# Optimization experiments

Measured on AMD Instinct MI355X. Metric: run time of the kernel, lower is better.

Reference implementation:

```python
import jax, jax.numpy as jnp
import numpy as np
from jax import lax

K = 9      # 3x3 kernel points
PAD = 1
EPS = 1e-5

def _conv3x3(x, w):
    # x: [B,C,H,W], w: [O,C,3,3] -> [B,O,H,W], stride 1, pad 1
    return lax.conv_general_dilated(x, w, (1, 1), [(PAD, PAD), (PAD, PAD)],
                                    dimension_numbers=('NCHW', 'OIHW', 'NCHW'))

def _bilinear_sample(x, py, px):
    # x: [B,C,H,W]; py,px: [B,K,H,W] float sample coords -> [B,C,K,H,W]
    # Zero padding outside bounds (mmcv deform_conv semantics).
    B, C, H, W = x.shape
    y0 = jnp.floor(py)
    x0 = jnp.floor(px)
    wy1 = py - y0
    wx1 = px - x0
    xf = x.reshape(B, C, H * W)

    def corner(yc, xc, wgt):
        valid = (yc >= 0) & (yc <= H - 1) & (xc >= 0) & (xc <= W - 1)
        yi = jnp.clip(yc, 0, H - 1).astype(jnp.int32)
        xi = jnp.clip(xc, 0, W - 1).astype(jnp.int32)
        idx = (yi * W + xi).reshape(B, -1)                       # [B, K*H*W]
        v = jax.vmap(lambda f, i: jnp.take(f, i, axis=1))(xf, idx)  # [B,C,K*H*W]
        v = v.reshape(B, C, K, H, W)
        return v * jnp.where(valid, wgt, 0.0)[:, None]

    return (corner(y0,     x0,     (1 - wy1) * (1 - wx1))
          + corner(y0,     x0 + 1, (1 - wy1) * wx1)
          + corner(y0 + 1, x0,     wy1 * (1 - wx1))
          + corner(y0 + 1, x0 + 1, wy1 * wx1))

def _dcn_bn_relu(x, w_off, b_off, w, gamma, beta, mean, var):
    B, C, H, W = x.shape
    # offset conv: [B, 2K, H, W]; channel pairs are (dy, dx) per kernel point
    off = _conv3x3(x, w_off) + b_off[None, :, None, None]
    off = off.reshape(B, K, 2, H, W)
    dy, dx = off[:, :, 0], off[:, :, 1]
    kk = jnp.arange(K)
    ky = (kk // 3 - PAD).astype(x.dtype)   # kernel y deltas
    kx = (kk % 3 - PAD).astype(x.dtype)    # kernel x deltas
    py = dy + jnp.arange(H, dtype=x.dtype)[None, None, :, None] + ky[None, :, None, None]
    px = dx + jnp.arange(W, dtype=x.dtype)[None, None, None, :] + kx[None, :, None, None]
    s = _bilinear_sample(x, py, px)                       # [B,C,K,H,W]
    out = jnp.einsum('bckhw,ock->bohw', s, w.reshape(w.shape[0], C, K))
    # BatchNorm (eval stats) + ReLU
    inv = gamma * lax.rsqrt(var + EPS)
    return jax.nn.relu(out * inv[None, :, None, None]
                       + (beta - mean * inv)[None, :, None, None])

def setup_inputs() -> dict:
    key = jax.random.key(0)
    ks = jax.random.split(key, 8)
    B, Cin, Cout, H, W = 4, 64, 64, 128, 128
    fan = 1.0 / np.sqrt(Cin * K)
    return {
        'x':      jax.random.normal(ks[0], (B, Cin, H, W), jnp.float32),
        'w_off1': jax.random.normal(ks[1], (2 * K, Cin, 3, 3), jnp.float32) * 0.1,
        'b_off1': jnp.zeros((2 * K,), jnp.float32),
        'w1':     jax.random.normal(ks[2], (Cout, Cin, 3, 3), jnp.float32) * fan,
        'g1':     jnp.ones((Cout,), jnp.float32),
        'be1':    jnp.zeros((Cout,), jnp.float32),
        'm1':     jax.random.normal(ks[3], (Cout,), jnp.float32) * 0.01,
        'v1':     jnp.abs(jax.random.normal(ks[4], (Cout,), jnp.float32)) * 0.1 + 0.9,
        'w_off2': jax.random.normal(ks[5], (2 * K, Cout, 3, 3), jnp.float32) * 0.1,
        'b_off2': jnp.zeros((2 * K,), jnp.float32),
        'w2':     jax.random.normal(ks[6], (Cout, Cout, 3, 3), jnp.float32) * fan,
        'g2':     jnp.ones((Cout,), jnp.float32),
        'be2':    jnp.zeros((Cout,), jnp.float32),
        'm2':     jax.random.normal(ks[7], (Cout,), jnp.float32) * 0.01,
        'v2':     jnp.ones((Cout,), jnp.float32),
    }

def reference(x, w_off1, b_off1, w1, g1, be1, m1, v1,
              w_off2, b_off2, w2, g2, be2, m2, v2):
    h = _dcn_bn_relu(x, w_off1, b_off1, w1, g1, be1, m1, v1)
    return _dcn_bn_relu(h, w_off2, b_off2, w2, g2, be2, m2, v2)
```

## Files before the change

kernel.cpp:

```cpp
#include <hip/hip_runtime.h>

#define BAR_LGKM()                                         \
  do {                                                     \
    asm volatile("s_waitcnt lgkmcnt(0)" ::: "memory");     \
    __builtin_amdgcn_s_barrier();                          \
  } while (0)

__device__ __forceinline__ int swz_block(int bid) {
  return ((bid & 7) << 7) + (bid >> 3);
}


__global__ __launch_bounds__(256) void prep_kernel(
    const float* __restrict__ w1, const float* __restrict__ w2,
    const float* __restrict__ woff1, const float* __restrict__ woff2,
    const float* __restrict__ g1, const float* __restrict__ be1,
    const float* __restrict__ m1, const float* __restrict__ v1,
    const float* __restrict__ g2, const float* __restrict__ be2,
    const float* __restrict__ m2, const float* __restrict__ v2,
    float* __restrict__ ws) {
  float* wt1 = ws;
  float* wt2 = ws + 36864;
  float* wo1 = ws + 73728;
  float* wo2 = ws + 84096;
  float* bn1 = ws + 94464;
  float* bn2 = ws + 94592;
  int idx = blockIdx.x * 256 + threadIdx.x;
  if (idx < 73728) {
    int t = (idx < 36864) ? idx : idx - 36864;
    const float* w = (idx < 36864) ? w1 : w2;
    float* wt = (idx < 36864) ? wt1 : wt2;
    int oi = t & 7;
    int rest = t >> 3;
    int k = rest % 9;
    int cog = rest / 9;
    int og = cog & 7, c = cog >> 3;
    int o = og * 8 + oi;
    wt[t] = w[(o * 64 + c) * 9 + k];
  } else if (idx < 94464) {
    int u = idx - 73728;
    int t2 = (u < 10368) ? u : u - 10368;
    const float* w = (u < 10368) ? woff1 : woff2;
    float* wo = (u < 10368) ? wo1 : wo2;
    int j = t2 % 18;
    int v = t2 / 18;
    int tt = v % 9;
    int c = v / 9;
    wo[t2] = w[(j * 64 + c) * 9 + tt];
  } else if (idx < 94528) {
    int o = idx - 94464;
    float s = g1[o] * rsqrtf(v1[o] + 1e-5f);
    bn1[o] = s;
    bn1[64 + o] = be1[o] - m1[o] * s;
  } else if (idx < 94592) {
    int o = idx - 94528;
    float s = g2[o] * rsqrtf(v2[o] + 1e-5f);
    bn2[o] = s;
    bn2[64 + o] = be2[o] - m2[o] * s;
  }
}

__global__ __launch_bounds__(512, 8) void conv_off_kernel(
    const float* __restrict__ xin, const float* __restrict__ wofft,
    const float* __restrict__ boff, float* __restrict__ off) {
  __shared__ float halo[2][792];
  int tid = threadIdx.x;
  int pxl = tid & 63;
  int og = tid >> 6;
  int ogu = __builtin_amdgcn_readfirstlane(og);
  int p0 = swz_block(blockIdx.x) * 64;
  int b = p0 >> 14, hw0 = p0 & 16383;
  int h = hw0 >> 7, w0 = hw0 & 127;

  bool sv = tid < 396;
  int pp = (tid >= 198) ? 1 : 0;
  int pos = tid - pp * 198;
  int r = pos / 66, cc = pos - r * 66;
  int yy = h + r - 1, xx = w0 + cc - 1;
  bool inb = sv && (yy >= 0) && (yy < 128) && (xx >= 0) && (xx < 128);
  int ofs = (yy << 7) + xx;
  const float* xb0 = xin + ((size_t)(b * 64) << 14);

  float stg0 = inb ? xb0[((size_t)pp << 14) + ofs] : 0.f;
  float stg1 = inb ? xb0[((size_t)(2 + pp) << 14) + ofs] : 0.f;

  int jbase = (ogu < 2) ? ogu * 3 : 6 + (ogu - 2) * 2;
  int nj = (ogu < 2) ? 3 : 2;
  int jc2 = jbase + 2;
  if (jc2 > 17) jc2 = 17;

  float acc[3] = {0.f, 0.f, 0.f};

#pragma unroll 1
  for (int cg = 0; cg < 64; cg += 4) {
    int bufi = (cg >> 2) & 1;
    if (sv) {
      halo[bufi][pp * 198 + pos] = stg0;
      halo[bufi][(2 + pp) * 198 + pos] = stg1;
    }
    if (cg < 60) {
      stg0 = inb ? xb0[((size_t)(cg + 4 + pp) << 14) + ofs] : 0.f;
      stg1 = inb ? xb0[((size_t)(cg + 6 + pp) << 14) + ofs] : 0.f;
    }
    BAR_LGKM();
    const float* hb = halo[bufi];
#pragma unroll
    for (int p = 0; p < 4; ++p) {
      const float* wc = wofft + (cg + p) * 162;
#pragma unroll
      for (int t = 0; t < 9; ++t) {
        float v = hb[p * 198 + (t / 3) * 66 + pxl + (t % 3)];
        acc[0] = fmaf(v, wc[t * 18 + jbase], acc[0]);
        acc[1] = fmaf(v, wc[t * 18 + jbase + 1], acc[1]);
        acc[2] = fmaf(v, wc[t * 18 + jc2], acc[2]);
      }
    }
  }
#pragma unroll
  for (int i = 0; i < 3; ++i) {
    if (i < nj) {
      int j = jbase + i;
      off[((size_t)(b * 18 + j) << 14) + hw0 + pxl] = acc[i] + boff[j];
    }
  }
}

__global__ __launch_bounds__(512, 8) void dcn_main_kernel(
    const float* __restrict__ xin, const float* __restrict__ off,
    const float* __restrict__ wt, const float* __restrict__ bn,
    float* __restrict__ out) {
  __shared__ float sbuf[2][576];
  int tid = threadIdx.x;
  int pxl = tid & 63;
  int og = tid >> 6;
  int ogu = __builtin_amdgcn_readfirstlane(og);
  int p0 = swz_block(blockIdx.x) * 64;
  int b = p0 >> 14, hw0 = p0 & 16383;
  int h = hw0 >> 7, w0 = hw0 & 127;
  const float* xb = xin + ((size_t)b << 20);

  bool act1 = (tid & 7) == 0;
  int s1 = 512 + (tid >> 3);

  float pw0[4], pw1[4];
  int ra0, rb0, ra1, rb1;
  bool se0a, se1a, se0b, se1b;

#pragma unroll
  for (int j = 0; j < 2; ++j) {
    bool a = (j == 0) || act1;
    int s = (j == 0) ? tid : s1;
    int k = s >> 6;
    int pxs = s & 63;
    int hw = hw0 + pxs;
    float dy = a ? off[((size_t)(b * 18 + 2 * k) << 14) + hw] : 0.f;
    float dx = a ? off[((size_t)(b * 18 + 2 * k + 1) << 14) + hw] : 0.f;
    float py = (float)(h + k / 3 - 1) + dy;
    float pxf = (float)(w0 + pxs + k % 3 - 1) + dx;
    float y0f = floorf(py), x0f = floorf(pxf);
    float wy1 = py - y0f, wx1 = pxf - x0f;
    float wy0 = 1.f - wy1, wx0 = 1.f - wx1;
    int y0 = (int)y0f, x0 = (int)x0f;
    int y1 = y0 + 1, x1 = x0 + 1;
    bool vy0 = (y0 >= 0) && (y0 <= 127);
    bool vy1 = (y1 >= 0) && (y1 <= 127);
    bool vx0 = (x0 >= 0) && (x0 <= 127);
    bool vx1 = (x1 >= 0) && (x1 <= 127);
    float* pw = (j == 0) ? pw0 : pw1;
    pw[0] = (vy0 && vx0) ? wy0 * wx0 : 0.f;
    pw[1] = (vy0 && vx1) ? wy0 * wx1 : 0.f;
    pw[2] = (vy1 && vx0) ? wy1 * wx0 : 0.f;
    pw[3] = (vy1 && vx1) ? wy1 * wx1 : 0.f;
    int y0c = min(max(y0, 0), 127), y1c = min(max(y1, 0), 127);
    int xb2 = min(max(x0, 0), 126);
    if (j == 0) {
      ra0 = (y0c << 7) + xb2; rb0 = (y1c << 7) + xb2;
      se0a = (x0 == xb2); se1a = (x0 + 1 == xb2);
    } else {
      ra1 = (y0c << 7) + xb2; rb1 = (y1c << 7) + xb2;
      se0b = (x0 == xb2); se1b = (x0 + 1 == xb2);
    }
  }

  float2 A0, A1, A2, A3, B0, B1, B2, B3;
  A0 = *(const float2*)(xb + ra0);
  A1 = *(const float2*)(xb + rb0);
  A2 = act1 ? *(const float2*)(xb + ra1) : make_float2(0.f, 0.f);
  A3 = act1 ? *(const float2*)(xb + rb1) : make_float2(0.f, 0.f);
  {
    const float* x1p = xb + 16384;
    B0 = *(const float2*)(x1p + ra0);
    B1 = *(const float2*)(x1p + rb0);
    B2 = act1 ? *(const float2*)(x1p + ra1) : make_float2(0.f, 0.f);
    B3 = act1 ? *(const float2*)(x1p + rb1) : make_float2(0.f, 0.f);
  }

  float acc[8];
#pragma unroll
  for (int oi = 0; oi < 8; ++oi) acc[oi] = 0.f;

#pragma unroll 1
  for (int c = 0; c < 64; c += 2) {
    {
      float v00 = se0a ? A0.x : A0.y;
      float v01 = se1a ? A0.x : A0.y;
      float v10 = se0a ? A1.x : A1.y;
      float v11 = se1a ? A1.x : A1.y;
      sbuf[0][tid] = fmaf(pw0[0], v00,
                     fmaf(pw0[1], v01,
                     fmaf(pw0[2], v10, pw0[3] * v11)));
    }
    if (act1) {
      float v00 = se0b ? A2.x : A2.y;
      float v01 = se1b ? A2.x : A2.y;
      float v10 = se0b ? A3.x : A3.y;
      float v11 = se1b ? A3.x : A3.y;
      sbuf[0][s1] = fmaf(pw1[0], v00,
                    fmaf(pw1[1], v01,
                    fmaf(pw1[2], v10, pw1[3] * v11)));
    }
    if (c < 62) {
      const float* xn = xb + ((size_t)(c + 2) << 14);
      A0 = *(const float2*)(xn + ra0);
      A1 = *(const float2*)(xn + rb0);
      if (act1) {
        A2 = *(const float2*)(xn + ra1);
        A3 = *(const float2*)(xn + rb1);
      }
    }
    BAR_LGKM();
    {
      const float* wc = wt + (c * 8 + ogu) * 72;
#pragma unroll
      for (int k = 0; k < 9; ++k) {
        float sval = sbuf[0][k * 64 + pxl];
#pragma unroll
        for (int oi = 0; oi < 8; ++oi)
          acc[oi] = fmaf(sval, wc[k * 8 + oi], acc[oi]);
      }
    }
    {
      float v00 = se0a ? B0.x : B0.y;
      float v01 = se1a ? B0.x : B0.y;
      float v10 = se0a ? B1.x : B1.y;
      float v11 = se1a ? B1.x : B1.y;
      sbuf[1][tid] = fmaf(pw0[0], v00,
                     fmaf(pw0[1], v01,
                     fmaf(pw0[2], v10, pw0[3] * v11)));
    }
    if (act1) {
      float v00 = se0b ? B2.x : B2.y;
      float v01 = se1b ? B2.x : B2.y;
      float v10 = se0b ? B3.x : B3.y;
      float v11 = se1b ? B3.x : B3.y;
      sbuf[1][s1] = fmaf(pw1[0], v00,
                    fmaf(pw1[1], v01,
                    fmaf(pw1[2], v10, pw1[3] * v11)));
    }
    if (c < 61) {
      const float* xn = xb + ((size_t)(c + 3) << 14);
      B0 = *(const float2*)(xn + ra0);
      B1 = *(const float2*)(xn + rb0);
      if (act1) {
        B2 = *(const float2*)(xn + ra1);
        B3 = *(const float2*)(xn + rb1);
      }
    }
    BAR_LGKM();
    {
      const float* wc = wt + ((c + 1) * 8 + ogu) * 72;
#pragma unroll
      for (int k = 0; k < 9; ++k) {
        float sval = sbuf[1][k * 64 + pxl];
#pragma unroll
        for (int oi = 0; oi < 8; ++oi)
          acc[oi] = fmaf(sval, wc[k * 8 + oi], acc[oi]);
      }
    }
  }

#pragma unroll
  for (int oi = 0; oi < 8; ++oi) {
    int o = ogu * 8 + oi;
    float rres = fmaf(acc[oi], bn[o], bn[64 + o]);
    out[((size_t)(b * 64 + o) << 14) + hw0 + pxl] = fmaxf(rres, 0.f);
  }
}

extern "C" void kernel_launch(void* const* d_in, const int* in_sizes, int n_in,
                              void* d_out, int out_size, void* d_ws, size_t ws_size,
                              hipStream_t stream) {
  const float* x      = (const float*)d_in[0];
  const float* w_off1 = (const float*)d_in[1];
  const float* b_off1 = (const float*)d_in[2];
  const float* w1     = (const float*)d_in[3];
  const float* g1     = (const float*)d_in[4];
  const float* be1    = (const float*)d_in[5];
  const float* m1     = (const float*)d_in[6];
  const float* v1     = (const float*)d_in[7];
  const float* w_off2 = (const float*)d_in[8];
  const float* b_off2 = (const float*)d_in[9];
  const float* w2     = (const float*)d_in[10];
  const float* g2     = (const float*)d_in[11];
  const float* be2    = (const float*)d_in[12];
  const float* m2     = (const float*)d_in[13];
  const float* v2     = (const float*)d_in[14];
  float* out = (float*)d_out;

  float* ws   = (float*)d_ws;
  float* wt1  = ws;
  float* wt2  = ws + 36864;
  float* wo1  = ws + 73728;
  float* wo2  = ws + 84096;
  float* bn1  = ws + 94464;
  float* bn2  = ws + 94592;
  float* offb = ws + 94720;
  float* hbuf = ws + 1274368;

  prep_kernel<<<370, 256, 0, stream>>>(w1, w2, w_off1, w_off2,
                                       g1, be1, m1, v1, g2, be2, m2, v2, ws);

  conv_off_kernel<<<1024, 512, 0, stream>>>(x, wo1, b_off1, offb);
  dcn_main_kernel<<<1024, 512, 0, stream>>>(x, offb, wt1, bn1, hbuf);

  conv_off_kernel<<<1024, 512, 0, stream>>>(hbuf, wo2, b_off2, offb);
  dcn_main_kernel<<<1024, 512, 0, stream>>>(hbuf, offb, wt2, bn2, out);
}
```

Baseline: 386.9 us.

## Stage weights in LDS and merge channel pairs into one barrier per iteration

The main DCN kernel now double-buffers both the sampled values and the per-channel-pair weights in shared memory. Two channels are processed per iteration with one barrier instead of two. Weights are prefetched into registers and staged cooperatively, replacing the per-wave scalar global weight loads with float4 LDS reads. This cuts barrier count and scalar memory latency, at the cost of more LDS and more registers, which may lower occupancy under launch bounds of 512 threads with 8 blocks.

```diff
diff --git a/kernel.cpp b/kernel.cpp
--- a/kernel.cpp
+++ b/kernel.cpp
@@ -129,7 +129,8 @@
     const float* __restrict__ xin, const float* __restrict__ off,
     const float* __restrict__ wt, const float* __restrict__ bn,
     float* __restrict__ out) {
-  __shared__ float sbuf[2][576];
+  __shared__ __align__(16) float sS[2][1152];
+  __shared__ __align__(16) float sW[2][1152];
   int tid = threadIdx.x;
   int pxl = tid & 63;
   int og = tid >> 6;
@@ -141,6 +142,7 @@
 
   bool act1 = (tid & 7) == 0;
   int s1 = 512 + (tid >> 3);
+  bool wl = tid < 288;
 
   float pw0[4], pw1[4];
   int ra0, rb0, ra1, rb1;
@@ -194,6 +196,7 @@
     B2 = act1 ? *(const float2*)(x1p + ra1) : make_float2(0.f, 0.f);
     B3 = act1 ? *(const float2*)(x1p + rb1) : make_float2(0.f, 0.f);
   }
+  float4 wreg = wl ? *(const float4*)(wt + (tid << 2)) : make_float4(0, 0, 0, 0);
 
   float acc[8];
 #pragma unroll
@@ -201,23 +204,39 @@
 
 #pragma unroll 1
   for (int c = 0; c < 64; c += 2) {
+    int buf = (c >> 1) & 1;
+    if (wl) *(float4*)&sW[buf][tid << 2] = wreg;
     {
       float v00 = se0a ? A0.x : A0.y;
       float v01 = se1a ? A0.x : A0.y;
       float v10 = se0a ? A1.x : A1.y;
       float v11 = se1a ? A1.x : A1.y;
-      sbuf[0][tid] = fmaf(pw0[0], v00,
+      sS[buf][tid] = fmaf(pw0[0], v00,
                      fmaf(pw0[1], v01,
                      fmaf(pw0[2], v10, pw0[3] * v11)));
+      v00 = se0a ? B0.x : B0.y;
+      v01 = se1a ? B0.x : B0.y;
+      v10 = se0a ? B1.x : B1.y;
+      v11 = se1a ? B1.x : B1.y;
+      sS[buf][576 + tid] = fmaf(pw0[0], v00,
+                           fmaf(pw0[1], v01,
+                           fmaf(pw0[2], v10, pw0[3] * v11)));
     }
     if (act1) {
       float v00 = se0b ? A2.x : A2.y;
       float v01 = se1b ? A2.x : A2.y;
       float v10 = se0b ? A3.x : A3.y;
       float v11 = se1b ? A3.x : A3.y;
-      sbuf[0][s1] = fmaf(pw1[0], v00,
+      sS[buf][s1] = fmaf(pw1[0], v00,
                     fmaf(pw1[1], v01,
                     fmaf(pw1[2], v10, pw1[3] * v11)));
+      v00 = se0b ? B2.x : B2.y;
+      v01 = se1b ? B2.x : B2.y;
+      v10 = se0b ? B3.x : B3.y;
+      v11 = se1b ? B3.x : B3.y;
+      sS[buf][576 + s1] = fmaf(pw1[0], v00,
+                          fmaf(pw1[1], v01,
+                          fmaf(pw1[2], v10, pw1[3] * v11)));
     }
     if (c < 62) {
       const float* xn = xb + ((size_t)(c + 2) << 14);
@@ -227,54 +246,33 @@
         A2 = *(const float2*)(xn + ra1);
         A3 = *(const float2*)(xn + rb1);
       }
+      const float* xn2 = xn + 16384;
+      B0 = *(const float2*)(xn2 + ra0);
+      B1 = *(const float2*)(xn2 + rb0);
+      if (act1) {
+        B2 = *(const float2*)(xn2 + ra1);
+        B3 = *(const float2*)(xn2 + rb1);
+      }
+      if (wl) wreg = *(const float4*)(wt + (c + 2) * 576 + (tid << 2));
     }
     BAR_LGKM();
-    {
-      const float* wc = wt + (c * 8 + ogu) * 72;
+#pragma unroll
+    for (int p = 0; p < 2; ++p) {
+      const float* wb = &sW[buf][p * 576 + ogu * 72];
+      const float* sb = &sS[buf][p * 576 + pxl];
 #pragma unroll
       for (int k = 0; k < 9; ++k) {
-        float sval = sbuf[0][k * 64 + pxl];
-#pragma unroll
-        for (int oi = 0; oi < 8; ++oi)
-          acc[oi] = fmaf(sval, wc[k * 8 + oi], acc[oi]);
-      }
-    }
-    {
-      float v00 = se0a ? B0.x : B0.y;
-      float v01 = se1a ? B0.x : B0.y;
-      float v10 = se0a ? B1.x : B1.y;
-      float v11 = se1a ? B1.x : B1.y;
-      sbuf[1][tid] = fmaf(pw0[0], v00,
-                     fmaf(pw0[1], v01,
-                     fmaf(pw0[2], v10, pw0[3] * v11)));
-    }
-    if (act1) {
-      float v00 = se0b ? B2.x : B2.y;
-      float v01 = se1b ? B2.x : B2.y;
-      float v10 = se0b ? B3.x : B3.y;
-      float v11 = se1b ? B3.x : B3.y;
-      sbuf[1][s1] = fmaf(pw1[0], v00,
-                    fmaf(pw1[1], v01,
-                    fmaf(pw1[2], v10, pw1[3] * v11)));
-    }
-    if (c < 61) {
-      const float* xn = xb + ((size_t)(c + 3) << 14);
-      B0 = *(const float2*)(xn + ra0);
-      B1 = *(const float2*)(xn + rb0);
-      if (act1) {
-        B2 = *(const float2*)(xn + ra1);
-        B3 = *(const float2*)(xn + rb1);
-      }
-    }
-    BAR_LGKM();
-    {
-      const float* wc = wt + ((c + 1) * 8 + ogu) * 72;
-#pragma unroll
-      for (int k = 0; k < 9; ++k) {
-        float sval = sbuf[1][k * 64 + pxl];
-#pragma unroll
-        for (int oi = 0; oi < 8; ++oi)
-          acc[oi] = fmaf(sval, wc[k * 8 + oi], acc[oi]);
+        float4 wA = *(const float4*)(wb + k * 8);
+        float4 wB = *(const float4*)(wb + k * 8 + 4);
+        float sval = sb[k * 64];
+        acc[0] = fmaf(sval, wA.x, acc[0]);
+        acc[1] = fmaf(sval, wA.y, acc[1]);
+        acc[2] = fmaf(sval, wA.z, acc[2]);
+        acc[3] = fmaf(sval, wA.w, acc[3]);
+        acc[4] = fmaf(sval, wB.x, acc[4]);
+        acc[5] = fmaf(sval, wB.y, acc[5]);
+        acc[6] = fmaf(sval, wB.z, acc[6]);
+        acc[7] = fmaf(sval, wB.w, acc[7]);
       }
     }
   }
```

New measurement: 1.105 ms. 186% more time.
